# Performance work log

Measured on AMD Instinct MI355X. Metric: run time of the kernel, lower is better.

## Reference

```python
import jax, jax.numpy as jnp
import numpy as np

B, S, D = 4, 1024, 1024
H = 16
HD = D // H  # head_dim = 64


def setup_inputs() -> dict:
    key = jax.random.key(0)
    k1, k2, k3 = jax.random.split(key, 3)
    x = jax.random.normal(k1, (B, S, D), dtype=jnp.float32)
    # qkv_proj: Linear(input_dim, 3*embed_dim), stored as (in, out) for x @ W
    scale = 1.0 / np.sqrt(D)
    W_qkv = jax.random.uniform(k2, (D, 3 * D), dtype=jnp.float32, minval=-scale, maxval=scale)
    b_qkv = jax.random.uniform(k3, (3 * D,), dtype=jnp.float32, minval=-scale, maxval=scale)
    return {"x": x, "W_qkv": W_qkv, "b_qkv": b_qkv}


def reference(x, W_qkv, b_qkv):
    b, s, _ = x.shape
    qkv = x @ W_qkv + b_qkv                       # [B,S,3D]
    qkv = qkv.reshape(b, s, H, 3 * HD)            # [B,S,H,3*hd]
    qkv = qkv.transpose(0, 2, 1, 3)               # [B,H,S,3*hd]
    q, k, v = jnp.split(qkv, 3, axis=-1)          # each [B,H,S,hd]
    scores = jnp.einsum('bhqd,bhkd->bhqk', q, k) / jnp.sqrt(jnp.float32(HD))
    attn = jax.nn.softmax(scores, axis=-1)        # [B,H,S,S]
    out = jnp.einsum('bhqk,bhkd->bhqd', attn, v)  # [B,H,S,hd]
    values = out.transpose(0, 2, 1, 3).reshape(b, s, H * HD)  # [B,S,D]
    return values
```

## Files before the change

kernel.cpp:

```cpp
#include <hip/hip_runtime.h>
#include <hip/hip_bf16.h>
#include <stdint.h>

#define BATCH 4
#define SEQ 1024
#define DMODEL 1024
#define NH 16
#define HD 64

typedef __attribute__((ext_vector_type(8))) short short8;
typedef __attribute__((ext_vector_type(4))) float f32x4;

__device__ __forceinline__ unsigned short f2bf(float f) {
    union { float f; uint32_t u; } v; v.f = f;
    uint32_t r = v.u + 0x7fff + ((v.u >> 16) & 1);
    return (unsigned short)(r >> 16);
}

__device__ __forceinline__ uint32_t pack2bf(float lo, float hi) {
    return (uint32_t)f2bf(lo) | ((uint32_t)f2bf(hi) << 16);
}

__device__ __forceinline__ void async_copy16(const unsigned short* g, unsigned short* l) {
    __builtin_amdgcn_global_load_lds(
        (__attribute__((address_space(1))) void*)g,
        (__attribute__((address_space(3))) void*)l,
        16, 0, 0);
}

__global__ __launch_bounds__(256) void prep_kernel(const float* __restrict__ x,
                                                   const float* __restrict__ W,
                                                   unsigned short* __restrict__ xb,
                                                   unsigned short* __restrict__ Wt) {
    __shared__ float tile[32][33];
    int bid = blockIdx.x;
    if (bid < 2048) {
        int t = bid * 256 + threadIdx.x;
        const float4* p = (const float4*)x + (size_t)t * 2;
        float4 a = p[0], b = p[1];
        short8 o;
        o[0] = (short)f2bf(a.x); o[1] = (short)f2bf(a.y);
        o[2] = (short)f2bf(a.z); o[3] = (short)f2bf(a.w);
        o[4] = (short)f2bf(b.x); o[5] = (short)f2bf(b.y);
        o[6] = (short)f2bf(b.z); o[7] = (short)f2bf(b.w);
        *((short8*)xb + t) = o;
    } else {
        int r = bid - 2048;
        int nb = (r % 96) * 32;
        int kb = (r / 96) * 32;
        int tx = threadIdx.x & 31;
        int ty = threadIdx.x >> 5;
#pragma unroll
        for (int i = 0; i < 4; i++) {
            int k = kb + ty + i * 8;
            tile[ty + i * 8][tx] = W[(size_t)k * 3072 + nb + tx];
        }
        __syncthreads();
#pragma unroll
        for (int i = 0; i < 4; i++) {
            int n = nb + ty + i * 8;
            Wt[(size_t)n * 1024 + kb + tx] = f2bf(tile[tx][ty + i * 8]);
        }
    }
}

#define BM 128
#define BN 128
#define BKK 64

__global__ __launch_bounds__(256) void qkv_gemm_kernel(
    const unsigned short* __restrict__ xb,
    const unsigned short* __restrict__ wt,
    const float* __restrict__ bias,
    unsigned short* __restrict__ Qb,
    unsigned short* __restrict__ Kb,
    unsigned short* __restrict__ VbT)
{
    __shared__ __align__(16) unsigned short As[BM][64];
    __shared__ __align__(16) unsigned short Bs[BN][64];
    int tid = threadIdx.x;
    int wave = tid >> 6, lane = tid & 63;
    int quad = lane >> 4, l16 = lane & 15;
    int wm = wave >> 1, wn = wave & 1;
    int m0 = blockIdx.x * BM;
    int n0 = blockIdx.y * BN;

    int grow = lane >> 3;
    int gcol = ((lane & 7) ^ grow) << 3;
    const unsigned short* gA = xb + (size_t)(m0 + wave * 32 + grow) * 1024 + gcol;
    const unsigned short* gB = wt + (size_t)(n0 + wave * 32 + grow) * 1024 + gcol;
    unsigned short* ldsA = &As[wave * 32][0];
    unsigned short* ldsB = &Bs[wave * 32][0];
    int sw = l16 & 7;

    f32x4 acc[4][4] = {};
    for (int k0 = 0; k0 < 1024; k0 += BKK) {
        __syncthreads();
#pragma unroll
        for (int i = 0; i < 4; i++) {
            async_copy16(gA + (size_t)i * 8 * 1024 + k0, ldsA + i * 512);
            async_copy16(gB + (size_t)i * 8 * 1024 + k0, ldsB + i * 512);
        }
        __syncthreads();
#pragma unroll
        for (int kk = 0; kk < BKK; kk += 32) {
            int kb = kk >> 3;
            short8 af[4], bf[4];
#pragma unroll
            for (int t = 0; t < 4; t++) {
                int ar = wm * 64 + t * 16 + l16;
                af[t] = *(const short8*)&As[ar][((kb + quad) ^ sw) << 3];
            }
#pragma unroll
            for (int t = 0; t < 4; t++) {
                int br = wn * 64 + t * 16 + l16;
                bf[t] = *(const short8*)&Bs[br][((kb + quad) ^ sw) << 3];
            }
#pragma unroll
            for (int mt = 0; mt < 4; mt++)
#pragma unroll
                for (int nt = 0; nt < 4; nt++)
                    acc[mt][nt] = __builtin_amdgcn_mfma_f32_16x16x32_bf16(
                        af[mt], bf[nt], acc[mt][nt], 0, 0, 0);
        }
    }
#pragma unroll
    for (int nt = 0; nt < 4; nt++) {
        int n = n0 + wn * 64 + nt * 16 + l16;
        int h = n / 192;
        int c = n - h * 192;
        int which = c >> 6;
        int d = c & 63;
        float bv = bias[n];
        float sc = (which == 0) ? 0.125f : 1.0f;
#pragma unroll
        for (int mt = 0; mt < 4; mt++) {
#pragma unroll
            for (int r = 0; r < 4; r++) {
                int m = m0 + wm * 64 + mt * 16 + quad * 4 + r;
                int b = m >> 10, s = m & 1023;
                float v = (acc[mt][nt][r] + bv) * sc;
                unsigned short bf_v = f2bf(v);
                int bh = b * 16 + h;
                if (which == 2) {
                    VbT[((size_t)bh * 64 + d) * 1024 + s] = bf_v;
                } else {
                    unsigned short* dst = (which == 0) ? Qb : Kb;
                    dst[((size_t)bh * 1024 + s) * 64 + d] = bf_v;
                }
            }
        }
    }
}

#define BQ 128
#define BKV 128

__global__ __launch_bounds__(256, 2) void attn_kernel(
    const unsigned short* __restrict__ Qb,
    const unsigned short* __restrict__ Kb,
    const unsigned short* __restrict__ VbT,
    float* __restrict__ out)
{
    __shared__ unsigned short Qs[BQ][64];
    __shared__ unsigned short Ks[BKV][64];
    __shared__ unsigned short Vts[HD][128];

    int tid = threadIdx.x;
    int wave = tid >> 6, lane = tid & 63;
    int quad = lane >> 4, l16 = lane & 15;

    int id = blockIdx.x;
    int xcd = id & 7, rest = id >> 3;
    int qt = rest & 7, grp = rest >> 3;
    int bh = grp * 8 + xcd;
    int q0 = qt * BQ;

    const unsigned short* Qp = Qb + (size_t)bh * SEQ * HD;
    const unsigned short* Kp = Kb + (size_t)bh * SEQ * HD;
    const unsigned short* Vp = VbT + (size_t)bh * HD * SEQ;

    int f_q = (l16 & 3) | (((l16 >> 3) & 1) << 2);
    int f_k = (l16 & 3) | (((l16 >> 2) & 1) << 2);
    int f_v = l16 & 7;
    int rbase = ((l16 >> 2) << 3) | (l16 & 3);

#pragma unroll
    for (int i = 0; i < 4; i++) {
        int idx = i * 256 + tid;
        int row = idx >> 3, pb = idx & 7;
        int fr = (row & 3) | (((row >> 3) & 1) << 2);
        int lb = pb ^ fr;
        *(short8*)&Qs[row][pb * 8] = *(const short8*)&Qp[(size_t)(q0 + row) * HD + lb * 8];
    }

    f32x4 oacc[2][4] = {};
    float lsum[2] = {0.f, 0.f};

    for (int kt = 0; kt < SEQ; kt += BKV) {
        __syncthreads();
#pragma unroll
        for (int i = 0; i < 4; i++) {
            int idx = i * 256 + tid;
            int krow = idx >> 3, kpb = idx & 7;
            int kfr = (krow & 3) | (((krow >> 3) & 1) << 2);
            int klb = kpb ^ kfr;
            *(short8*)&Ks[krow][kpb * 8] = *(const short8*)&Kp[(size_t)(kt + krow) * HD + klb * 8];
            int vrow = idx >> 4, vpb = idx & 15;
            int vlb = vpb ^ (vrow & 7);
            *(short8*)&Vts[vrow][vpb * 8] = *(const short8*)&Vp[(size_t)vrow * SEQ + kt + vlb * 8];
        }
        __syncthreads();

        f32x4 sacc[2][8] = {};
#pragma unroll
        for (int ds_ = 0; ds_ < HD; ds_ += 32) {
            int k0b = ds_ >> 3;
            short8 qf[2];
#pragma unroll
            for (int g = 0; g < 2; g++)
                qf[g] = *(const short8*)&Qs[wave * 32 + g * 16 + l16][((k0b + quad) ^ f_q) * 8];
#pragma unroll
            for (int nt = 0; nt < 8; nt++) {
                int krow = rbase + ((nt >> 1) << 5) + ((nt & 1) << 2);
                short8 kf = *(const short8*)&Ks[krow][((k0b + quad) ^ f_k) * 8];
#pragma unroll
                for (int g = 0; g < 2; g++)
                    sacc[g][nt] = __builtin_amdgcn_mfma_f32_16x16x32_bf16(kf, qf[g], sacc[g][nt], 0, 0, 0);
            }
        }

        uint32_t u[2][8][2];
#pragma unroll
        for (int g = 0; g < 2; g++)
#pragma unroll
            for (int nt = 0; nt < 8; nt++) {
                float p0 = __expf(sacc[g][nt][0]);
                float p1 = __expf(sacc[g][nt][1]);
                float p2 = __expf(sacc[g][nt][2]);
                float p3 = __expf(sacc[g][nt][3]);
                lsum[g] += (p0 + p1) + (p2 + p3);
                u[g][nt][0] = pack2bf(p0, p1);
                u[g][nt][1] = pack2bf(p2, p3);
            }

#pragma unroll
        for (int c = 0; c < 4; c++) {
            short8 vf[4];
#pragma unroll
            for (int nt = 0; nt < 4; nt++)
                vf[nt] = *(const short8*)&Vts[nt * 16 + l16][(((c << 2) + quad) ^ f_v) * 8];
#pragma unroll
            for (int g = 0; g < 2; g++) {
                union { uint32_t w[4]; short8 s; } pf;
                pf.w[0] = u[g][2 * c][0];
                pf.w[1] = u[g][2 * c][1];
                pf.w[2] = u[g][2 * c + 1][0];
                pf.w[3] = u[g][2 * c + 1][1];
#pragma unroll
                for (int nt = 0; nt < 4; nt++)
                    oacc[g][nt] = __builtin_amdgcn_mfma_f32_16x16x32_bf16(vf[nt], pf.s, oacc[g][nt], 0, 0, 0);
            }
        }
    }

#pragma unroll
    for (int g = 0; g < 2; g++) {
        lsum[g] += __shfl_xor(lsum[g], 16, 64);
        lsum[g] += __shfl_xor(lsum[g], 32, 64);
    }

    int b = bh >> 4, h = bh & 15;
#pragma unroll
    for (int g = 0; g < 2; g++) {
        float inv = 1.f / lsum[g];
        int s = q0 + wave * 32 + g * 16 + l16;
#pragma unroll
        for (int nt = 0; nt < 4; nt++) {
            float4 o;
            o.x = oacc[g][nt][0] * inv;
            o.y = oacc[g][nt][1] * inv;
            o.z = oacc[g][nt][2] * inv;
            o.w = oacc[g][nt][3] * inv;
            *(float4*)&out[(size_t)(b * SEQ + s) * DMODEL + h * HD + nt * 16 + quad * 4] = o;
        }
    }
}

extern "C" void kernel_launch(void* const* d_in, const int* in_sizes, int n_in,
                              void* d_out, int out_size, void* d_ws, size_t ws_size,
                              hipStream_t stream) {
    const float* x    = (const float*)d_in[0];
    const float* W    = (const float*)d_in[1];
    const float* bias = (const float*)d_in[2];
    float* out = (float*)d_out;
    char* ws = (char*)d_ws;

    unsigned short* xb  = (unsigned short*)(ws);
    unsigned short* wt  = (unsigned short*)(ws + 8388608);
    unsigned short* Qb  = (unsigned short*)(ws + 14680064);
    unsigned short* Kb  = (unsigned short*)(ws + 23068672);
    unsigned short* VbT = (unsigned short*)(ws + 31457280);

    prep_kernel<<<5120, 256, 0, stream>>>(x, W, xb, wt);
    dim3 gg(32, 24);
    qkv_gemm_kernel<<<gg, 256, 0, stream>>>(xb, wt, bias, Qb, Kb, VbT);
    attn_kernel<<<512, 256, 0, stream>>>(Qb, Kb, VbT, out);
}
```

Baseline: 159.1 us.

## Register-prefetch next K tile in GEMM and attention, vectorize V stores

The QKV GEMM drops global_load_lds async copies and instead prefetches the next K-slice into registers while the current slice is computed, then writes those registers to LDS at the start of the next iteration. The attention kernel does the same register prefetch for its K and V tiles. The V-transpose epilogue now writes four consecutive bf16 values as one vector store. Both kernels raise launch_bounds occupancy to 3 blocks per CU, which adds register pressure on top of the extra prefetch registers and risks spills.

```diff
diff --git a/kernel.cpp b/kernel.cpp
--- a/kernel.cpp
+++ b/kernel.cpp
@@ -10,6 +10,7 @@
 
 typedef __attribute__((ext_vector_type(8))) short short8;
 typedef __attribute__((ext_vector_type(4))) float f32x4;
+typedef __attribute__((ext_vector_type(4))) unsigned short ushort4v;
 
 __device__ __forceinline__ unsigned short f2bf(float f) {
     union { float f; uint32_t u; } v; v.f = f;
@@ -19,13 +20,6 @@
 
 __device__ __forceinline__ uint32_t pack2bf(float lo, float hi) {
     return (uint32_t)f2bf(lo) | ((uint32_t)f2bf(hi) << 16);
-}
-
-__device__ __forceinline__ void async_copy16(const unsigned short* g, unsigned short* l) {
-    __builtin_amdgcn_global_load_lds(
-        (__attribute__((address_space(1))) void*)g,
-        (__attribute__((address_space(3))) void*)l,
-        16, 0, 0);
 }
 
 __global__ __launch_bounds__(256) void prep_kernel(const float* __restrict__ x,
@@ -68,7 +62,7 @@
 #define BN 128
 #define BKK 64
 
-__global__ __launch_bounds__(256) void qkv_gemm_kernel(
+__global__ __launch_bounds__(256, 3) void qkv_gemm_kernel(
     const unsigned short* __restrict__ xb,
     const unsigned short* __restrict__ wt,
     const float* __restrict__ bias,
@@ -89,19 +83,33 @@
     int gcol = ((lane & 7) ^ grow) << 3;
     const unsigned short* gA = xb + (size_t)(m0 + wave * 32 + grow) * 1024 + gcol;
     const unsigned short* gB = wt + (size_t)(n0 + wave * 32 + grow) * 1024 + gcol;
-    unsigned short* ldsA = &As[wave * 32][0];
-    unsigned short* ldsB = &Bs[wave * 32][0];
+    unsigned short* ldsA = &As[wave * 32][0] + lane * 8;
+    unsigned short* ldsB = &Bs[wave * 32][0] + lane * 8;
     int sw = l16 & 7;
+
+    short8 areg[4], breg[4];
+#pragma unroll
+    for (int i = 0; i < 4; i++) {
+        areg[i] = *(const short8*)(gA + (size_t)i * 8 * 1024);
+        breg[i] = *(const short8*)(gB + (size_t)i * 8 * 1024);
+    }
 
     f32x4 acc[4][4] = {};
     for (int k0 = 0; k0 < 1024; k0 += BKK) {
         __syncthreads();
 #pragma unroll
         for (int i = 0; i < 4; i++) {
-            async_copy16(gA + (size_t)i * 8 * 1024 + k0, ldsA + i * 512);
-            async_copy16(gB + (size_t)i * 8 * 1024 + k0, ldsB + i * 512);
-        }
-        __syncthreads();
+            *(short8*)(ldsA + i * 512) = areg[i];
+            *(short8*)(ldsB + i * 512) = breg[i];
+        }
+        __syncthreads();
+        if (k0 + BKK < 1024) {
+#pragma unroll
+            for (int i = 0; i < 4; i++) {
+                areg[i] = *(const short8*)(gA + (size_t)i * 8 * 1024 + k0 + BKK);
+                breg[i] = *(const short8*)(gB + (size_t)i * 8 * 1024 + k0 + BKK);
+            }
+        }
 #pragma unroll
         for (int kk = 0; kk < BKK; kk += 32) {
             int kb = kk >> 3;
@@ -132,21 +140,28 @@
         int which = c >> 6;
         int d = c & 63;
         float bv = bias[n];
-        float sc = (which == 0) ? 0.125f : 1.0f;
-#pragma unroll
-        for (int mt = 0; mt < 4; mt++) {
-#pragma unroll
-            for (int r = 0; r < 4; r++) {
-                int m = m0 + wm * 64 + mt * 16 + quad * 4 + r;
+        if (which == 2) {
+#pragma unroll
+            for (int mt = 0; mt < 4; mt++) {
+                int m = m0 + wm * 64 + mt * 16 + quad * 4;
                 int b = m >> 10, s = m & 1023;
-                float v = (acc[mt][nt][r] + bv) * sc;
-                unsigned short bf_v = f2bf(v);
-                int bh = b * 16 + h;
-                if (which == 2) {
-                    VbT[((size_t)bh * 64 + d) * 1024 + s] = bf_v;
-                } else {
-                    unsigned short* dst = (which == 0) ? Qb : Kb;
-                    dst[((size_t)bh * 1024 + s) * 64 + d] = bf_v;
+                ushort4v o;
+                o[0] = f2bf(acc[mt][nt][0] + bv);
+                o[1] = f2bf(acc[mt][nt][1] + bv);
+                o[2] = f2bf(acc[mt][nt][2] + bv);
+                o[3] = f2bf(acc[mt][nt][3] + bv);
+                *(ushort4v*)&VbT[((size_t)((b * 16 + h) * 64 + d)) * 1024 + s] = o;
+            }
+        } else {
+            unsigned short* dst = (which == 0) ? Qb : Kb;
+            float sc = (which == 0) ? 0.125f : 1.0f;
+#pragma unroll
+            for (int mt = 0; mt < 4; mt++) {
+#pragma unroll
+                for (int r = 0; r < 4; r++) {
+                    int m = m0 + wm * 64 + mt * 16 + quad * 4 + r;
+                    int b = m >> 10, s = m & 1023;
+                    dst[((size_t)((b * 16 + h) * 1024 + s)) * 64 + d] = f2bf((acc[mt][nt][r] + bv) * sc);
                 }
             }
         }
@@ -156,7 +171,7 @@
 #define BQ 128
 #define BKV 128
 
-__global__ __launch_bounds__(256, 2) void attn_kernel(
+__global__ __launch_bounds__(256, 3) void attn_kernel(
     const unsigned short* __restrict__ Qb,
     const unsigned short* __restrict__ Kb,
     const unsigned short* __restrict__ VbT,
@@ -194,6 +209,21 @@
         *(short8*)&Qs[row][pb * 8] = *(const short8*)&Qp[(size_t)(q0 + row) * HD + lb * 8];
     }
 
+    short8 kreg[4], vreg[4];
+    auto load_tile = [&](int kt) {
+#pragma unroll
+        for (int i = 0; i < 4; i++) {
+            int idx = i * 256 + tid;
+            int krow = idx >> 3, kpb = idx & 7;
+            int klb = kpb ^ ((krow & 3) | (((krow >> 3) & 1) << 2));
+            kreg[i] = *(const short8*)&Kp[(size_t)(kt + krow) * HD + klb * 8];
+            int vrow = idx >> 4, vpb = idx & 15;
+            int vlb = vpb ^ (vrow & 7);
+            vreg[i] = *(const short8*)&Vp[(size_t)vrow * SEQ + kt + vlb * 8];
+        }
+    };
+    load_tile(0);
+
     f32x4 oacc[2][4] = {};
     float lsum[2] = {0.f, 0.f};
 
@@ -203,14 +233,12 @@
         for (int i = 0; i < 4; i++) {
             int idx = i * 256 + tid;
             int krow = idx >> 3, kpb = idx & 7;
-            int kfr = (krow & 3) | (((krow >> 3) & 1) << 2);
-            int klb = kpb ^ kfr;
-            *(short8*)&Ks[krow][kpb * 8] = *(const short8*)&Kp[(size_t)(kt + krow) * HD + klb * 8];
+            *(short8*)&Ks[krow][kpb * 8] = kreg[i];
             int vrow = idx >> 4, vpb = idx & 15;
-            int vlb = vpb ^ (vrow & 7);
-            *(short8*)&Vts[vrow][vpb * 8] = *(const short8*)&Vp[(size_t)vrow * SEQ + kt + vlb * 8];
-        }
-        __syncthreads();
+            *(short8*)&Vts[vrow][vpb * 8] = vreg[i];
+        }
+        __syncthreads();
+        if (kt + BKV < SEQ) load_tile(kt + BKV);
 
         f32x4 sacc[2][8] = {};
 #pragma unroll
```

New measurement: 161.2 us. No clear change (+1.3%).
